# Optimization experiments

Hardware: AMD Instinct MI355X
Metric: run time of the kernel (lower is better)

Reference implementation:

```python
import jax, jax.numpy as jnp
import numpy as np

N_PRIORS = 262144
N_CLASSES = 81  # includes background at index 0


def _decode(loc, priors, variance):
    # Standard SSD decode: priors are [N,4] (cx, cy, w, h) in relative coords.
    centers = priors[:, :2] + loc[:, :2] * variance[0] * priors[:, 2:]
    sizes = priors[:, 2:] * jnp.exp(loc[:, 2:] * variance[1])
    mins = centers - sizes * 0.5          # (xmin, ymin)
    maxs = mins + sizes                   # (xmax, ymax)
    return jnp.concatenate([mins, maxs], axis=-1)  # [N,4]


def setup_inputs() -> dict:
    key = jax.random.key(0)
    k1, k2, k3 = jax.random.split(key, 3)
    inp = jax.random.normal(k1, (1, N_PRIORS, 4 + N_CLASSES), dtype=jnp.float32)
    cxy = jax.random.uniform(k2, (N_PRIORS, 2), dtype=jnp.float32)
    wh = jax.random.uniform(k3, (N_PRIORS, 2), dtype=jnp.float32) * 0.1 + 0.05
    priors = jnp.concatenate([cxy, wh], axis=-1)
    variance = jnp.array([0.1, 0.2], dtype=jnp.float32)
    score_threshold = jnp.array([0.3], dtype=jnp.float32)
    return {"input": inp, "priors": priors, "variance": variance,
            "score_threshold": score_threshold}


def reference(input, priors, variance, score_threshold):
    # input: [1, N, 4+C]
    loc = input[0, :, :4]                                   # [N,4]
    cls = jax.nn.softmax(input[0, :, 4:], axis=-1)          # [N,C]
    class_conf = jnp.max(cls, axis=1)                       # [N]
    class_pred = jnp.argmax(cls, axis=1)                    # [N] int
    boxes = _decode(loc, priors, variance)                  # [N,4]
    # torch version compacts via nonzero/index_select; jit-compatible
    # equivalent: keep fixed length N and mask out invalid rows.
    valid = (class_pred > 0) & (class_conf > score_threshold[0])  # [N] bool
    boxes = jnp.where(valid[:, None], boxes, 0.0)
    class_conf = jnp.where(valid, class_conf, 0.0)
    class_pred_out = jnp.where(valid, class_pred - 1, -1)
    detections = jnp.concatenate(
        [boxes, class_conf[:, None], class_pred_out[:, None].astype(jnp.float32)],
        axis=-1)                                            # [N,6]
    return boxes, class_conf, class_pred_out, detections[None]
```

## Files before the change

kernel.cpp:

```cpp
#include <hip/hip_runtime.h>
#include <cmath>

#define NCLS 81
#define ROW  (4 + NCLS)

__global__ __launch_bounds__(256) void ssd_decode_kernel(
    const float* __restrict__ inp,
    const float* __restrict__ priors,
    const float* __restrict__ var,
    const float* __restrict__ thr,
    float* __restrict__ out,
    int n)
{
    int i = blockIdx.x * 256 + threadIdx.x;
    if (i >= n) return;

    const float* row = inp + (long long)i * ROW;

    float l0 = row[0], l1 = row[1], l2 = row[2], l3 = row[3];

    float e[NCLS];
#pragma unroll
    for (int c = 0; c < NCLS; ++c) e[c] = row[4 + c];

    float m = e[0];
#pragma unroll
    for (int c = 1; c < NCLS; ++c) m = fmaxf(m, e[c]);

#pragma unroll
    for (int c = 0; c < NCLS; ++c) e[c] = (float)exp((double)(e[c] - m));

    float r0=e[0], r1=e[1], r2=e[2], r3=e[3], r4=e[4], r5=e[5], r6=e[6], r7=e[7];
#pragma unroll
    for (int c = 8; c < 80; c += 8) {
        r0 += e[c+0]; r1 += e[c+1]; r2 += e[c+2]; r3 += e[c+3];
        r4 += e[c+4]; r5 += e[c+5]; r6 += e[c+6]; r7 += e[c+7];
    }
    float s = ((r0 + r1) + (r2 + r3)) + ((r4 + r5) + (r6 + r7));
    s += e[80];

    float pm = -1.0f;
    int am = 0;
#pragma unroll
    for (int c = 0; c < NCLS; ++c) {
        float p = e[c] / s;
        if (p > pm) { pm = p; am = c; }
    }
    float conf = pm;

    float4 pr = reinterpret_cast<const float4*>(priors)[i];
    float v0 = var[0], v1 = var[1];
    float cx = pr.x + l0 * v0 * pr.z;
    float cy = pr.y + l1 * v0 * pr.w;
    float w  = pr.z * expf(l2 * v1);
    float h  = pr.w * expf(l3 * v1);
    float x0 = cx - w * 0.5f;
    float y0 = cy - h * 0.5f;
    float x1 = x0 + w;
    float y1 = y0 + h;

    bool valid = (am > 0) && (conf > thr[0]);

    float4 box;
    box.x = valid ? x0 : 0.0f;
    box.y = valid ? y0 : 0.0f;
    box.z = valid ? x1 : 0.0f;
    box.w = valid ? y1 : 0.0f;
    float cz = valid ? conf : 0.0f;
    float pz = valid ? (float)(am - 1) : -1.0f;

    reinterpret_cast<float4*>(out)[i] = box;
    out[(long long)4 * n + i] = cz;
    out[(long long)5 * n + i] = pz;
    float* det = out + (long long)6 * n + (long long)i * 6;
    float2* det2 = reinterpret_cast<float2*>(det);
    det2[0] = make_float2(box.x, box.y);
    det2[1] = make_float2(box.z, box.w);
    det2[2] = make_float2(cz, pz);
}

extern "C" void kernel_launch(void* const* d_in, const int* in_sizes, int n_in,
                              void* d_out, int out_size, void* d_ws, size_t ws_size,
                              hipStream_t stream)
{
    const float* inp    = (const float*)d_in[0];
    const float* priors = (const float*)d_in[1];
    const float* var    = (const float*)d_in[2];
    const float* thr    = (const float*)d_in[3];
    float* out = (float*)d_out;

    int n = in_sizes[1] / 4;
    int blocks = (n + 255) / 256;
    ssd_decode_kernel<<<blocks, 256, 0, stream>>>(inp, priors, var, thr, out, n);
}
```

Before: 146.5 us.

## Stage rows through LDS with coalesced float4 loads and custom exp

Each block now copies its 128 input rows into shared memory with coalesced float4 loads, replacing per-thread strided row reads from global memory. The double-precision library exp is replaced by an inline polynomial exp in double, and the argmax is found by comparing against a threshold derived from 1/s instead of dividing every class by the sum. This trades about 43KB of LDS per block (which limits occupancy) for much better global memory coalescing. It also removes the tail bounds check, so it assumes n is a multiple of 128.

Measured after the change: 158.9 us. 8.5% more time.

```diff
diff --git a/kernel.cpp b/kernel.cpp
--- a/kernel.cpp
+++ b/kernel.cpp
@@ -1,10 +1,36 @@
 #include <hip/hip_runtime.h>
-#include <cmath>
 
 #define NCLS 81
-#define ROW  (4 + NCLS)
+#define ROW  85
+#define TPB  128
 
-__global__ __launch_bounds__(256) void ssd_decode_kernel(
+__device__ __forceinline__ float exp_cr(float xf) {
+    double x = (double)xf;
+    x = (x < -150.0) ? -150.0 : x;
+    double t = x * 1.4426950408889634074;
+    double nd = rint(t);
+    double r = fma(nd, -6.93147180369123816490e-01, x);
+    r = fma(nd, -1.90821492927058770002e-10, r);
+    double p = 1.0 / 6227020800.0;
+    p = fma(p, r, 1.0 / 479001600.0);
+    p = fma(p, r, 1.0 / 39916800.0);
+    p = fma(p, r, 1.0 / 3628800.0);
+    p = fma(p, r, 1.0 / 362880.0);
+    p = fma(p, r, 1.0 / 40320.0);
+    p = fma(p, r, 1.0 / 5040.0);
+    p = fma(p, r, 1.0 / 720.0);
+    p = fma(p, r, 1.0 / 120.0);
+    p = fma(p, r, 1.0 / 24.0);
+    p = fma(p, r, 1.0 / 6.0);
+    p = fma(p, r, 0.5);
+    p = fma(p, r, 1.0);
+    p = fma(p, r, 1.0);
+    long long ni = (long long)nd;
+    double sc = __longlong_as_double((1023LL + ni) << 52);
+    return (float)(p * sc);
+}
+
+__global__ __launch_bounds__(TPB) void ssd_decode_kernel(
     const float* __restrict__ inp,
     const float* __restrict__ priors,
     const float* __restrict__ var,
@@ -12,68 +38,94 @@
     float* __restrict__ out,
     int n)
 {
-    int i = blockIdx.x * 256 + threadIdx.x;
-    if (i >= n) return;
+    __shared__ __align__(16) float lds[TPB * ROW];
+    const int tid = threadIdx.x;
+    const long long base = (long long)blockIdx.x * TPB;
+    if (base >= n) return;
 
-    const float* row = inp + (long long)i * ROW;
+    {
+        const float4* g4 = reinterpret_cast<const float4*>(inp) + base * ROW / 4;
+        float4* l4 = reinterpret_cast<float4*>(lds);
+        const int NV4 = TPB * ROW / 4;
+        #pragma unroll
+        for (int k = 0; k < NV4 / TPB; ++k)
+            l4[k * TPB + tid] = g4[k * TPB + tid];
+        const int tail = NV4 - (NV4 / TPB) * TPB;
+        if (tid < tail)
+            l4[(NV4 / TPB) * TPB + tid] = g4[(NV4 / TPB) * TPB + tid];
+    }
+    __syncthreads();
+
+    float* row = lds + tid * ROW;
+
+    float mx[8];
+    #pragma unroll
+    for (int j = 0; j < 8; ++j) mx[j] = row[4 + j];
+    #pragma unroll
+    for (int k = 1; k < 10; ++k)
+        #pragma unroll
+        for (int j = 0; j < 8; ++j) mx[j] = fmaxf(mx[j], row[4 + k * 8 + j]);
+    float m = fmaxf(fmaxf(fmaxf(mx[0], mx[1]), fmaxf(mx[2], mx[3])),
+                    fmaxf(fmaxf(mx[4], mx[5]), fmaxf(mx[6], mx[7])));
+    m = fmaxf(m, row[84]);
+
+    float racc[8];
+    #pragma unroll
+    for (int j = 0; j < 8; ++j) racc[j] = 0.0f;
+    #pragma unroll
+    for (int k = 0; k < 10; ++k)
+        #pragma unroll
+        for (int j = 0; j < 8; ++j) {
+            float e = exp_cr(row[4 + k * 8 + j] - m);
+            row[4 + k * 8 + j] = e;
+            racc[j] += e;
+        }
+    float s = ((racc[0] + racc[1]) + (racc[2] + racc[3]))
+            + ((racc[4] + racc[5]) + (racc[6] + racc[7]));
+    float e80 = exp_cr(row[84] - m);
+    row[84] = e80;
+    s += e80;
+
+    float pmax = 1.0f / s;
+    float t = 1.0f;
+    #pragma unroll
+    for (int k = 0; k < 8; ++k) {
+        float tn = __uint_as_float(__float_as_uint(t) - 1u);
+        t = ((tn / s) == pmax) ? tn : t;
+    }
+
+    int am = 81;
+    #pragma unroll
+    for (int c = 80; c >= 0; --c)
+        am = (row[4 + c] >= t) ? c : am;
 
     float l0 = row[0], l1 = row[1], l2 = row[2], l3 = row[3];
-
-    float e[NCLS];
-#pragma unroll
-    for (int c = 0; c < NCLS; ++c) e[c] = row[4 + c];
-
-    float m = e[0];
-#pragma unroll
-    for (int c = 1; c < NCLS; ++c) m = fmaxf(m, e[c]);
-
-#pragma unroll
-    for (int c = 0; c < NCLS; ++c) e[c] = (float)exp((double)(e[c] - m));
-
-    float r0=e[0], r1=e[1], r2=e[2], r3=e[3], r4=e[4], r5=e[5], r6=e[6], r7=e[7];
-#pragma unroll
-    for (int c = 8; c < 80; c += 8) {
-        r0 += e[c+0]; r1 += e[c+1]; r2 += e[c+2]; r3 += e[c+3];
-        r4 += e[c+4]; r5 += e[c+5]; r6 += e[c+6]; r7 += e[c+7];
-    }
-    float s = ((r0 + r1) + (r2 + r3)) + ((r4 + r5) + (r6 + r7));
-    s += e[80];
-
-    float pm = -1.0f;
-    int am = 0;
-#pragma unroll
-    for (int c = 0; c < NCLS; ++c) {
-        float p = e[c] / s;
-        if (p > pm) { pm = p; am = c; }
-    }
-    float conf = pm;
-
-    float4 pr = reinterpret_cast<const float4*>(priors)[i];
+    float4 pr = reinterpret_cast<const float4*>(priors)[base + tid];
     float v0 = var[0], v1 = var[1];
     float cx = pr.x + l0 * v0 * pr.z;
     float cy = pr.y + l1 * v0 * pr.w;
-    float w  = pr.z * expf(l2 * v1);
-    float h  = pr.w * expf(l3 * v1);
+    float w  = pr.z * exp_cr(l2 * v1);
+    float h  = pr.w * exp_cr(l3 * v1);
     float x0 = cx - w * 0.5f;
     float y0 = cy - h * 0.5f;
     float x1 = x0 + w;
     float y1 = y0 + h;
 
-    bool valid = (am > 0) && (conf > thr[0]);
+    bool valid = (am > 0) && (pmax > thr[0]);
 
     float4 box;
     box.x = valid ? x0 : 0.0f;
     box.y = valid ? y0 : 0.0f;
     box.z = valid ? x1 : 0.0f;
     box.w = valid ? y1 : 0.0f;
-    float cz = valid ? conf : 0.0f;
+    float cz = valid ? pmax : 0.0f;
     float pz = valid ? (float)(am - 1) : -1.0f;
 
+    const long long i = base + tid;
     reinterpret_cast<float4*>(out)[i] = box;
     out[(long long)4 * n + i] = cz;
     out[(long long)5 * n + i] = pz;
-    float* det = out + (long long)6 * n + (long long)i * 6;
-    float2* det2 = reinterpret_cast<float2*>(det);
+    float2* det2 = reinterpret_cast<float2*>(out + (long long)6 * n + i * 6);
     det2[0] = make_float2(box.x, box.y);
     det2[1] = make_float2(box.z, box.w);
     det2[2] = make_float2(cz, pz);
@@ -90,6 +142,6 @@
     float* out = (float*)d_out;
 
     int n = in_sizes[1] / 4;
-    int blocks = (n + 255) / 256;
-    ssd_decode_kernel<<<blocks, 256, 0, stream>>>(inp, priors, var, thr, out, n);
+    int blocks = (n + TPB - 1) / TPB;
+    ssd_decode_kernel<<<blocks, TPB, 0, stream>>>(inp, priors, var, thr, out, n);
 }
```
